# Performance work log

Measured on AMD Instinct MI355X. Metric: run time of the kernel, lower is better.

The kernel has to match this reference:

```python
import jax, jax.numpy as jnp
import numpy as np

B, N, E, H = 4, 512, 512, 8
HD = E // H // 2            # 32; per-head value dim is 2*HD = 64
C_IN = 64                   # u_proj Conv2d in_channels
LAMBDA_INIT = 0.8 - 0.6 * float(np.exp(-0.3 * (28.0 / 28.0) * (1 - 1)))  # layer_idx=1, depth=28 -> 0.2
LN_EPS = 1e-5


def setup_inputs() -> dict:
    key = jax.random.key(0)
    ks = jax.random.split(key, 13)
    x = jax.random.normal(ks[0], (B, N, E), dtype=jnp.float32)
    u = jax.random.normal(ks[1], (B, N, N, C_IN), dtype=jnp.float32)
    umask = jax.random.randint(ks[2], (B, N, N, 2 * H), 0, 2).astype(bool)
    s = 0.02
    v_w = jax.random.normal(ks[3], (E, E), dtype=jnp.float32) * s        # nn.Linear weight [out,in]
    out_w = jax.random.normal(ks[4], (E, E), dtype=jnp.float32) * s
    uproj_w = jax.random.normal(ks[5], (2 * H, C_IN), dtype=jnp.float32) * s  # 1x1 conv kernel
    uproj_b = jax.random.normal(ks[6], (2 * H,), dtype=jnp.float32) * s
    lq1 = jax.random.normal(ks[7], (E,), dtype=jnp.float32) * 0.1
    lk1 = jax.random.normal(ks[8], (E,), dtype=jnp.float32) * 0.1
    lq2 = jax.random.normal(ks[9], (E,), dtype=jnp.float32) * 0.1
    lk2 = jax.random.normal(ks[10], (E,), dtype=jnp.float32) * 0.1
    ln_w = jnp.ones((2 * HD,), dtype=jnp.float32)
    ln_b = jnp.zeros((2 * HD,), dtype=jnp.float32)
    return {"x": x, "u": u, "umask": umask, "v_w": v_w, "out_w": out_w,
            "uproj_w": uproj_w, "uproj_b": uproj_b,
            "lq1": lq1, "lk1": lk1, "lq2": lq2, "lk2": lk2,
            "ln_w": ln_w, "ln_b": ln_b}


def reference(x, u, umask, v_w, out_w, uproj_w, uproj_b, lq1, lk1, lq2, lk2, ln_w, ln_b):
    b, n, e = x.shape
    # v projection -> [B, H, N, 2*HD]
    v = jnp.einsum('bne,fe->bnf', x, v_w).reshape(b, n, H, 2 * HD).transpose(0, 2, 1, 3)
    # 1x1 conv on u: [B,N,N,C_IN] -> [B,N,N,2H]
    ue = jnp.einsum('bnmc,hc->bnmh', u, uproj_w) + uproj_b
    ue = jnp.where(umask, -jnp.inf, ue)
    # transpose(3,1): [B,N,N,2H] -> [B,2H,N,N]; softmax over last (key) axis
    aw = jax.nn.softmax(jnp.transpose(ue, (0, 3, 2, 1)), axis=-1)
    lam1 = jnp.exp(jnp.sum(lq1 * lk1))
    lam2 = jnp.exp(jnp.sum(lq2 * lk2))
    lam = lam1 - lam2 + LAMBDA_INIT
    aw = aw.reshape(b, H, 2, n, n)
    diff = aw[:, :, 0] - lam * aw[:, :, 1]          # [B,H,N,N]
    attn = jnp.einsum('bhnm,bhmd->bhnd', diff, v)   # [B,H,N,2HD]
    # sub-LayerNorm over last dim
    mu = jnp.mean(attn, axis=-1, keepdims=True)
    var = jnp.mean(jnp.square(attn - mu), axis=-1, keepdims=True)
    attn = (attn - mu) * jax.lax.rsqrt(var + LN_EPS) * ln_w + ln_b
    attn = attn.transpose(0, 2, 1, 3).reshape(b, n, e)
    return jnp.einsum('bne,fe->bnf', attn, out_w)
```

## Files before the change

### kernel.cpp

```cpp
#include <hip/hip_runtime.h>
#include <math.h>

typedef _Float16 f16x8 __attribute__((ext_vector_type(8)));
typedef _Float16 f16x4 __attribute__((ext_vector_type(4)));
typedef float    f32x4 __attribute__((ext_vector_type(4)));

constexpr int kB  = 4;
constexpr int kN  = 512;
constexpr int kE  = 512;
constexpr int kH  = 8;
constexpr int kH2 = 16;
constexpr int kC  = 64;
constexpr int kDV = 64;
constexpr float kLamInit = 0.2f;

__global__ __launch_bounds__(256) void prep_kernel(
    const float* __restrict__ x, const float* __restrict__ vw,
    const float* __restrict__ ow,
    const float* __restrict__ lq1, const float* __restrict__ lk1,
    const float* __restrict__ lq2, const float* __restrict__ lk2,
    _Float16* __restrict__ x16, _Float16* __restrict__ w16v,
    _Float16* __restrict__ w16o, float* __restrict__ lam_out) {
  const int bid = blockIdx.x;
  if (bid < 1536) {
    const float* src; _Float16* dst; int base;
    if (bid < 1024)      { src = x;  dst = x16;  base = bid; }
    else if (bid < 1280) { src = vw; dst = w16v; base = bid - 1024; }
    else                 { src = ow; dst = w16o; base = bid - 1280; }
    const int i = base * 256 + threadIdx.x;
    const float4 v = ((const float4*)src)[i];
    union { _Float16 h[4]; uint2 u2; } P;
    P.h[0]=(_Float16)v.x; P.h[1]=(_Float16)v.y;
    P.h[2]=(_Float16)v.z; P.h[3]=(_Float16)v.w;
    *(uint2*)(dst + i * 4) = P.u2;
  } else if (threadIdx.x < 64) {
    float s1 = 0.f, s2 = 0.f;
    for (int i = threadIdx.x; i < kE; i += 64) { s1 += lq1[i]*lk1[i]; s2 += lq2[i]*lk2[i]; }
    #pragma unroll
    for (int o = 32; o; o >>= 1) { s1 += __shfl_xor(s1, o); s2 += __shfl_xor(s2, o); }
    if (threadIdx.x == 0) lam_out[0] = expf(s1) - expf(s2) + kLamInit;
  }
}

__global__ __launch_bounds__(256) void hgemmT_v(const _Float16* __restrict__ W16,
                                                const _Float16* __restrict__ X16,
                                                _Float16* __restrict__ Vt) {
  const int tid = threadIdx.x, lane = tid & 63, wv = tid >> 6;
  const int l15 = lane & 15, l4 = lane >> 4;
  const int f0 = blockIdx.y * 64 + wv * 16;
  const int n0 = blockIdx.x * 64;
  f32x4 acc[4] = {{0,0,0,0},{0,0,0,0},{0,0,0,0},{0,0,0,0}};
  const _Float16* Ap = W16 + (size_t)(f0 + l15) * kE + l4 * 8;
  const _Float16* Bp = X16 + (size_t)(n0 + l15) * kE + l4 * 8;
  for (int k0 = 0; k0 < kE; k0 += 32) {
    const f16x8 af = *(const f16x8*)(Ap + k0);
    #pragma unroll
    for (int t = 0; t < 4; ++t) {
      const f16x8 bf = *(const f16x8*)(Bp + (size_t)t * 16 * kE + k0);
      acc[t] = __builtin_amdgcn_mfma_f32_16x16x32_f16(af, bf, acc[t], 0, 0, 0);
    }
  }
  #pragma unroll
  for (int t = 0; t < 4; ++t)
    #pragma unroll
    for (int r = 0; r < 4; ++r) {
      const int f  = f0 + l4 * 4 + r;
      const int ng = n0 + t * 16 + l15;
      const int bb = ng >> 9, n = ng & 511;
      Vt[(((size_t)((bb * kH + (f >> 6)) * kDV) + (f & 63)) * kN) + n] = (_Float16)acc[t][r];
    }
}

__global__ __launch_bounds__(512, 4) void fused_attn4(
    const float* __restrict__ u, const int* __restrict__ umask,
    const float* __restrict__ uw, const float* __restrict__ ub,
    const _Float16* __restrict__ Vt,
    _Float16* __restrict__ Opart, float* __restrict__ Spart) {
  __shared__ _Float16 P[16 * 648];
  __shared__ float S_lds[8][16][17];
  const int tid = threadIdx.x, lane = tid & 63, wv = tid >> 6;
  const int l15 = lane & 15, l4 = lane >> 4;
  const int qt = blockIdx.x, kh = blockIdx.y, b = blockIdx.z;
  const int q0 = qt * 16;
  const int kstart = kh * 128;

  f16x8 bfrag[2];
  #pragma unroll
  for (int ch = 0; ch < 2; ++ch) {
    const float* wp = uw + l15 * 64 + ch * 32 + l4 * 8;
    const float4 wa = *(const float4*)wp;
    const float4 wb = *(const float4*)(wp + 4);
    f16x8 bf;
    bf[0]=(_Float16)wa.x; bf[1]=(_Float16)wa.y; bf[2]=(_Float16)wa.z; bf[3]=(_Float16)wa.w;
    bf[4]=(_Float16)wb.x; bf[5]=(_Float16)wb.y; bf[6]=(_Float16)wb.z; bf[7]=(_Float16)wb.w;
    bfrag[ch] = bf;
  }
  const float bias = ub[l15];

  float s_acc[4] = {};
  f32x4 oacc[2][4];
  #pragma unroll
  for (int s = 0; s < 2; ++s)
    #pragma unroll
    for (int d = 0; d < 4; ++d) oacc[s][d] = (f32x4){0,0,0,0};

  for (int t = 0; t < 4; ++t) {
    const int k0 = kstart + t * 32;
    _Float16 vals[4][4];
    #pragma unroll
    for (int kk = 0; kk < 4; ++kk) {
      const int k = k0 + wv * 4 + kk;
      const float* up = u + (((size_t)(b * kN + k)) * kN + q0 + l15) * kC + l4 * 8;
      f32x4 acc = {0.f, 0.f, 0.f, 0.f};
      #pragma unroll
      for (int ch = 0; ch < 2; ++ch) {
        const float4 a0 = *(const float4*)(up + ch * 32);
        const float4 a1 = *(const float4*)(up + ch * 32 + 4);
        f16x8 af;
        af[0]=(_Float16)a0.x; af[1]=(_Float16)a0.y; af[2]=(_Float16)a0.z; af[3]=(_Float16)a0.w;
        af[4]=(_Float16)a1.x; af[5]=(_Float16)a1.y; af[6]=(_Float16)a1.z; af[7]=(_Float16)a1.w;
        acc = __builtin_amdgcn_mfma_f32_16x16x32_f16(af, bfrag[ch], acc, 0, 0, 0);
      }
      const int* mrow = umask + (((size_t)(b * kN + k)) * kN + q0) * kH2 + l15;
      #pragma unroll
      for (int r = 0; r < 4; ++r) {
        const float e = mrow[(l4 * 4 + r) * kH2] ? 0.f : __expf(acc[r] + bias);
        s_acc[r] += e;
        vals[r][kk] = (_Float16)e;
      }
    }
    #pragma unroll
    for (int r = 0; r < 4; ++r) {
      union { _Float16 h[4]; uint2 u2; } PK;
      #pragma unroll
      for (int kk = 0; kk < 4; ++kk) PK.h[kk] = vals[r][kk];
      *(uint2*)&P[l15 * 648 + (l4 * 4 + r) * 40 + wv * 4] = PK.u2;
    }
    __syncthreads();
    f16x8 va[4];
    #pragma unroll
    for (int dt = 0; dt < 4; ++dt)
      va[dt] = *(const f16x8*)(Vt + (((size_t)((b * kH + wv) * kDV + dt * 16 + l15)) * kN) + k0 + l4 * 8);
    #pragma unroll
    for (int s = 0; s < 2; ++s) {
      const f16x8 pb = *(const f16x8*)&P[(wv * 2 + s) * 648 + l15 * 40 + l4 * 8];
      #pragma unroll
      for (int dt = 0; dt < 4; ++dt)
        oacc[s][dt] = __builtin_amdgcn_mfma_f32_16x16x32_f16(va[dt], pb, oacc[s][dt], 0, 0, 0);
    }
    __syncthreads();
  }

  #pragma unroll
  for (int r = 0; r < 4; ++r) S_lds[wv][l15][l4 * 4 + r] = s_acc[r];
  __syncthreads();
  const int blk = (b * 4 + kh) * 32 + qt;
  if (tid < 256) {
    const int h2 = tid >> 4, q = tid & 15;
    float S = 0.f;
    #pragma unroll
    for (int j = 0; j < 8; ++j) S += S_lds[j][h2][q];
    Spart[(size_t)blk * 256 + h2 * 16 + q] = S;
  }
  _Float16* ob = Opart + (size_t)blk * 16384;
  #pragma unroll
  for (int s = 0; s < 2; ++s)
    #pragma unroll
    for (int dt = 0; dt < 4; ++dt)
      #pragma unroll
      for (int r = 0; r < 4; ++r)
        ob[((size_t)(s * 8 + wv) * 64 + dt * 16 + l4 * 4 + r) * 16 + l15] =
            (_Float16)oacc[s][dt][r];
}

__global__ __launch_bounds__(256) void combine_out(
    const _Float16* __restrict__ Opart, const float* __restrict__ Spart,
    const float* __restrict__ lam_p, const float* __restrict__ ln_w,
    const float* __restrict__ ln_b, const _Float16* __restrict__ w16o,
    float* __restrict__ out) {
  __shared__ _Float16 a_lds[16][520];
  __shared__ float vsh[64][17];
  __shared__ float inv_sh[2][16];
  const int tid = threadIdx.x;
  const int fh = blockIdx.x, qt = blockIdx.y, b = blockIdx.z;
  const float lam = lam_p[0];

  for (int h = 0; h < 8; ++h) {
    if (tid < 32) {
      const int s = tid >> 4, q = tid & 15;
      float S = 0.f;
      #pragma unroll
      for (int kh = 0; kh < 4; ++kh)
        S += Spart[(size_t)((b * 4 + kh) * 32 + qt) * 256 + (h * 2 + s) * 16 + q];
      inv_sh[s][q] = (s ? lam : 1.0f) / S;
    }
    float a0[4] = {}, a1[4] = {};
    #pragma unroll
    for (int kh = 0; kh < 4; ++kh) {
      const size_t base = (size_t)((b * 4 + kh) * 32 + qt) * 16384;
      const f16x4 p0 = *(const f16x4*)(Opart + base + (size_t)(0 * 8 + h) * 1024 + tid * 4);
      const f16x4 p1 = *(const f16x4*)(Opart + base + (size_t)(1 * 8 + h) * 1024 + tid * 4);
      #pragma unroll
      for (int j = 0; j < 4; ++j) { a0[j] += (float)p0[j]; a1[j] += (float)p1[j]; }
    }
    __syncthreads();
    {
      const int d = tid >> 2, q0i = (tid & 3) * 4;
      #pragma unroll
      for (int j = 0; j < 4; ++j)
        vsh[d][q0i + j] = a0[j] * inv_sh[0][q0i + j] - a1[j] * inv_sh[1][q0i + j];
    }
    __syncthreads();
    const int q = tid >> 4, i = tid & 15;
    float vv[4], s1 = 0.f, s2 = 0.f;
    #pragma unroll
    for (int jj = 0; jj < 4; ++jj) {
      vv[jj] = vsh[i * 4 + jj][q];
      s1 += vv[jj]; s2 += vv[jj] * vv[jj];
    }
    #pragma unroll
    for (int o = 1; o < 16; o <<= 1) { s1 += __shfl_xor(s1, o); s2 += __shfl_xor(s2, o); }
    const float mu = s1 * (1.0f / kDV);
    const float var = s2 * (1.0f / kDV) - mu * mu;
    const float rstd = rsqrtf(var + 1e-5f);
    #pragma unroll
    for (int jj = 0; jj < 4; ++jj)
      a_lds[q][h * kDV + i * 4 + jj] =
          (_Float16)((vv[jj] - mu) * rstd * ln_w[i * 4 + jj] + ln_b[i * 4 + jj]);
  }
  __syncthreads();

  const int lane = tid & 63, wv = tid >> 6;
  const int l15 = lane & 15, l4 = lane >> 4;
  const int f0 = fh * 256 + wv * 64;
  f32x4 acc[4] = {{0,0,0,0},{0,0,0,0},{0,0,0,0},{0,0,0,0}};
  const _Float16* Wp = w16o + (size_t)(f0 + l15) * kE + l4 * 8;
  for (int k0 = 0; k0 < kE; k0 += 32) {
    const f16x8 af = *(const f16x8*)&a_lds[l15][k0 + l4 * 8];
    #pragma unroll
    for (int ft = 0; ft < 4; ++ft) {
      const f16x8 bf = *(const f16x8*)(Wp + (size_t)ft * 16 * kE + k0);
      acc[ft] = __builtin_amdgcn_mfma_f32_16x16x32_f16(af, bf, acc[ft], 0, 0, 0);
    }
  }
  #pragma unroll
  for (int ft = 0; ft < 4; ++ft)
    #pragma unroll
    for (int r = 0; r < 4; ++r)
      out[(size_t)(b * kN + qt * 16 + l4 * 4 + r) * kE + f0 + ft * 16 + l15] = acc[ft][r];
}

extern "C" void kernel_launch(void* const* d_in, const int* in_sizes, int n_in,
                              void* d_out, int out_size, void* d_ws, size_t ws_size,
                              hipStream_t stream) {
  const float* x     = (const float*)d_in[0];
  const float* u     = (const float*)d_in[1];
  const int*   umask = (const int*)d_in[2];
  const float* v_w   = (const float*)d_in[3];
  const float* out_w = (const float*)d_in[4];
  const float* uw    = (const float*)d_in[5];
  const float* ubias = (const float*)d_in[6];
  const float* lq1   = (const float*)d_in[7];
  const float* lk1   = (const float*)d_in[8];
  const float* lq2   = (const float*)d_in[9];
  const float* lk2   = (const float*)d_in[10];
  const float* ln_w  = (const float*)d_in[11];
  const float* ln_b  = (const float*)d_in[12];
  float* out = (float*)d_out;

  char* ws = (char*)d_ws;
  const size_t sz_half = (size_t)kB * kN * kE * 2;
  const size_t sz_w16  = (size_t)kE * kE * 2;
  const size_t sz_op   = (size_t)512 * 16384 * 2;
  const size_t sz_sp   = (size_t)512 * 256 * 4;
  const size_t off_x16 = 256;
  const size_t off_wv  = off_x16 + sz_half;
  const size_t off_wo  = off_wv + sz_w16;
  const size_t off_vt  = off_wo + sz_w16;
  const size_t off_op  = off_vt + sz_half;
  const size_t off_sp  = off_op + sz_op;
  if (ws_size < off_sp + sz_sp) return;
  float*    lam   = (float*)(ws);
  _Float16* x16   = (_Float16*)(ws + off_x16);
  _Float16* w16v  = (_Float16*)(ws + off_wv);
  _Float16* w16o  = (_Float16*)(ws + off_wo);
  _Float16* Vt    = (_Float16*)(ws + off_vt);
  _Float16* Opart = (_Float16*)(ws + off_op);
  float*    Spart = (float*)(ws + off_sp);

  prep_kernel<<<dim3(1537), dim3(256), 0, stream>>>(
      x, v_w, out_w, lq1, lk1, lq2, lk2, x16, w16v, w16o, lam);
  hgemmT_v<<<dim3(32, 8), dim3(256), 0, stream>>>(w16v, x16, Vt);
  fused_attn4<<<dim3(kN / 16, 4, kB), dim3(512), 0, stream>>>(
      u, umask, uw, ubias, Vt, Opart, Spart);
  combine_out<<<dim3(2, kN / 16, kB), dim3(256), 0, stream>>>(
      Opart, Spart, lam, ln_w, ln_b, w16o, out);
}
```

Before: 118.0 us.

## Pack umask into 16-bit head bitmasks in prep and prefetch them

The prep kernel gains extra blocks that read the int32 mask with coalesced int4 loads and pack the 16 per-head flags of each (b,k,q) entry into one 16-bit word in the workspace. The attention kernel then loads four such words per lane as a single 64-bit value and tests bits, instead of doing strided scalar int loads per row. It also prefetches the next tile's mask words during the PV stage. This replaces scattered, poorly coalesced mask reads in the hot kernel, at the cost of an extra pass over the full int32 mask plus an 8MB write and read.

```diff
diff --git a/kernel.cpp b/kernel.cpp
--- a/kernel.cpp
+++ b/kernel.cpp
@@ -14,13 +14,14 @@
 constexpr int kDV = 64;
 constexpr float kLamInit = 0.2f;
 
-__global__ __launch_bounds__(256) void prep_kernel(
+__global__ __launch_bounds__(256) void prep2_kernel(
     const float* __restrict__ x, const float* __restrict__ vw,
-    const float* __restrict__ ow,
+    const float* __restrict__ ow, const int* __restrict__ umask,
     const float* __restrict__ lq1, const float* __restrict__ lk1,
     const float* __restrict__ lq2, const float* __restrict__ lk2,
     _Float16* __restrict__ x16, _Float16* __restrict__ w16v,
-    _Float16* __restrict__ w16o, float* __restrict__ lam_out) {
+    _Float16* __restrict__ w16o, unsigned short* __restrict__ mbits,
+    float* __restrict__ lam_out) {
   const int bid = blockIdx.x;
   if (bid < 1536) {
     const float* src; _Float16* dst; int base;
@@ -33,12 +34,27 @@
     P.h[0]=(_Float16)v.x; P.h[1]=(_Float16)v.y;
     P.h[2]=(_Float16)v.z; P.h[3]=(_Float16)v.w;
     *(uint2*)(dst + i * 4) = P.u2;
-  } else if (threadIdx.x < 64) {
-    float s1 = 0.f, s2 = 0.f;
-    for (int i = threadIdx.x; i < kE; i += 64) { s1 += lq1[i]*lk1[i]; s2 += lq2[i]*lk2[i]; }
-    #pragma unroll
-    for (int o = 32; o; o >>= 1) { s1 += __shfl_xor(s1, o); s2 += __shfl_xor(s2, o); }
-    if (threadIdx.x == 0) lam_out[0] = expf(s1) - expf(s2) + kLamInit;
+  } else if (bid == 1536) {
+    if (threadIdx.x < 64) {
+      float s1 = 0.f, s2 = 0.f;
+      for (int i = threadIdx.x; i < kE; i += 64) { s1 += lq1[i]*lk1[i]; s2 += lq2[i]*lk2[i]; }
+      #pragma unroll
+      for (int o = 32; o; o >>= 1) { s1 += __shfl_xor(s1, o); s2 += __shfl_xor(s2, o); }
+      if (threadIdx.x == 0) lam_out[0] = expf(s1) - expf(s2) + kLamInit;
+    }
+  } else {
+    const int i = (bid - 1537) * 256 + threadIdx.x;
+    const int4* src = (const int4*)(umask + (size_t)i * kH2);
+    unsigned int w = 0;
+    #pragma unroll
+    for (int c = 0; c < 4; ++c) {
+      const int4 m = src[c];
+      w |= (m.x & 1) << (c * 4 + 0);
+      w |= (m.y & 1) << (c * 4 + 1);
+      w |= (m.z & 1) << (c * 4 + 2);
+      w |= (m.w & 1) << (c * 4 + 3);
+    }
+    mbits[i] = (unsigned short)w;
   }
 }
 
@@ -71,8 +87,8 @@
     }
 }
 
-__global__ __launch_bounds__(512, 4) void fused_attn4(
-    const float* __restrict__ u, const int* __restrict__ umask,
+__global__ __launch_bounds__(512, 4) void fused_attn8(
+    const float* __restrict__ u, const unsigned short* __restrict__ mbits,
     const float* __restrict__ uw, const float* __restrict__ ub,
     const _Float16* __restrict__ Vt,
     _Float16* __restrict__ Opart, float* __restrict__ Spart) {
@@ -97,12 +113,19 @@
   }
   const float bias = ub[l15];
 
+  const unsigned short* mb0 = mbits + (size_t)(b * kN) * kN + q0 + l4 * 4;
+
   float s_acc[4] = {};
   f32x4 oacc[2][4];
   #pragma unroll
   for (int s = 0; s < 2; ++s)
     #pragma unroll
     for (int d = 0; d < 4; ++d) oacc[s][d] = (f32x4){0,0,0,0};
+
+  unsigned long long pm[4];
+  #pragma unroll
+  for (int kk = 0; kk < 4; ++kk)
+    pm[kk] = *(const unsigned long long*)(mb0 + (size_t)(kstart + wv * 4 + kk) * kN);
 
   for (int t = 0; t < 4; ++t) {
     const int k0 = kstart + t * 32;
@@ -121,10 +144,9 @@
         af[4]=(_Float16)a1.x; af[5]=(_Float16)a1.y; af[6]=(_Float16)a1.z; af[7]=(_Float16)a1.w;
         acc = __builtin_amdgcn_mfma_f32_16x16x32_f16(af, bfrag[ch], acc, 0, 0, 0);
       }
-      const int* mrow = umask + (((size_t)(b * kN + k)) * kN + q0) * kH2 + l15;
       #pragma unroll
       for (int r = 0; r < 4; ++r) {
-        const float e = mrow[(l4 * 4 + r) * kH2] ? 0.f : __expf(acc[r] + bias);
+        const float e = ((pm[kk] >> (r * 16 + l15)) & 1ULL) ? 0.f : __expf(acc[r] + bias);
         s_acc[r] += e;
         vals[r][kk] = (_Float16)e;
       }
@@ -137,6 +159,11 @@
       *(uint2*)&P[l15 * 648 + (l4 * 4 + r) * 40 + wv * 4] = PK.u2;
     }
     __syncthreads();
+    if (t < 3) {
+      #pragma unroll
+      for (int kk = 0; kk < 4; ++kk)
+        pm[kk] = *(const unsigned long long*)(mb0 + (size_t)(k0 + 32 + wv * 4 + kk) * kN);
+    }
     f16x8 va[4];
     #pragma unroll
     for (int dt = 0; dt < 4; ++dt)
@@ -273,13 +300,15 @@
   const size_t sz_w16  = (size_t)kE * kE * 2;
   const size_t sz_op   = (size_t)512 * 16384 * 2;
   const size_t sz_sp   = (size_t)512 * 256 * 4;
+  const size_t sz_mb   = (size_t)kB * kN * kN * 2;
   const size_t off_x16 = 256;
   const size_t off_wv  = off_x16 + sz_half;
   const size_t off_wo  = off_wv + sz_w16;
   const size_t off_vt  = off_wo + sz_w16;
   const size_t off_op  = off_vt + sz_half;
   const size_t off_sp  = off_op + sz_op;
-  if (ws_size < off_sp + sz_sp) return;
+  const size_t off_mb  = off_sp + sz_sp;
+  if (ws_size < off_mb + sz_mb) return;
   float*    lam   = (float*)(ws);
   _Float16* x16   = (_Float16*)(ws + off_x16);
   _Float16* w16v  = (_Float16*)(ws + off_wv);
@@ -287,12 +316,13 @@
   _Float16* Vt    = (_Float16*)(ws + off_vt);
   _Float16* Opart = (_Float16*)(ws + off_op);
   float*    Spart = (float*)(ws + off_sp);
-
-  prep_kernel<<<dim3(1537), dim3(256), 0, stream>>>(
-      x, v_w, out_w, lq1, lk1, lq2, lk2, x16, w16v, w16o, lam);
+  unsigned short* mbits = (unsigned short*)(ws + off_mb);
+
+  prep2_kernel<<<dim3(5633), dim3(256), 0, stream>>>(
+      x, v_w, out_w, umask, lq1, lk1, lq2, lk2, x16, w16v, w16o, mbits, lam);
   hgemmT_v<<<dim3(32, 8), dim3(256), 0, stream>>>(w16v, x16, Vt);
-  fused_attn4<<<dim3(kN / 16, 4, kB), dim3(512), 0, stream>>>(
-      u, umask, uw, ubias, Vt, Opart, Spart);
+  fused_attn8<<<dim3(kN / 16, 4, kB), dim3(512), 0, stream>>>(
+      u, mbits, uw, ubias, Vt, Opart, Spart);
   combine_out<<<dim3(2, kN / 16, kB), dim3(256), 0, stream>>>(
       Opart, Spart, lam, ln_w, ln_b, w16o, out);
 }
```

New measurement: 111.2 us, median of 3. 5.8% less time.
